# Optimization experiments

Hardware: AMD Instinct MI355X
Metric: run time of the kernel (lower is better)

## Reference

```python
import jax, jax.numpy as jnp
import numpy as np

EPSILON = 1e-05


def setup_inputs() -> dict:
    key = jax.random.key(0)
    X = jax.random.normal(key, (4, 2048, 3), dtype=jnp.float32)
    K = jnp.ones((), dtype=jnp.float32)
    B = jnp.zeros((), dtype=jnp.float32)
    return {"X": X, "K": K, "B": B}


def reference(X, K, B):
    # X: [batch, N, D]
    delta_X = X[:, :, None, :] - X[:, None, :, :]          # [b, N, N, D]
    sq = jnp.sum(delta_X * delta_X, axis=-1, keepdims=True)  # [b, N, N, 1]
    # safe sqrt: distance is 0 on the diagonal; avoid nan-producing grad paths
    distance = jnp.sqrt(jnp.where(sq == 0, 1.0, sq))
    distance = jnp.where(sq == 0, 0.0, distance)
    direction = delta_X / (distance + EPSILON)
    force = (K * (distance - B)) * direction               # [b, N, N, D]
    aggregated_force = jnp.sum(force, axis=-2)             # [b, N, D]
    return X + aggregated_force
```

## Files before the change

kernel.cpp:

```cpp
#include <hip/hip_runtime.h>

#define NPTS 2048
#define NBATCH 4
#define TI 16
#define SJ 16
#define EPSF 1e-5f

__global__ __launch_bounds__(256) void spring_kernel(
    const float* __restrict__ X,
    const float* __restrict__ Kp,
    const float* __restrict__ Bp,
    float* __restrict__ out)
{
    __shared__ float xs[NPTS], ys[NPTS], zs[NPTS];

    const int tid = threadIdx.x;
    const int blocksPerBatch = NPTS / TI;
    const int b = blockIdx.x / blocksPerBatch;
    const int i_base = (blockIdx.x % blocksPerBatch) * TI;
    const float* Xb = X + b * (NPTS * 3);

    for (int e = tid; e < NPTS * 3; e += 256) {
        float v = Xb[e];
        int n = e / 3;
        int c = e - n * 3;
        if (c == 0)      xs[n] = v;
        else if (c == 1) ys[n] = v;
        else             zs[n] = v;
    }
    __syncthreads();

    const float K  = Kp[0];
    const float Bc = Bp[0];
    const float C  = K * (Bc + EPSF);

    const int il = tid >> 4;
    const int js = tid & 15;
    const int i  = i_base + il;

    const float xi = xs[i], yi = ys[i], zi = zs[i];

    float ax = 0.f, ay = 0.f, az = 0.f;
    #pragma unroll 8
    for (int j = js; j < NPTS; j += SJ) {
        float dx = xi - xs[j];
        float dy = yi - ys[j];
        float dz = zi - zs[j];
        float sq = dx*dx + dy*dy + dz*dz;
        float dist = __builtin_amdgcn_sqrtf(sq);
        float r = __builtin_amdgcn_rcpf(dist + EPSF);
        float s = fmaf(-C, r, K);
        ax = fmaf(dx, s, ax);
        ay = fmaf(dy, s, ay);
        az = fmaf(dz, s, az);
    }

    for (int d = 8; d > 0; d >>= 1) {
        ax += __shfl_down(ax, d, 16);
        ay += __shfl_down(ay, d, 16);
        az += __shfl_down(az, d, 16);
    }

    if (js == 0) {
        float* o = out + (b * NPTS + i) * 3;
        o[0] = xi + ax;
        o[1] = yi + ay;
        o[2] = zi + az;
    }
}

extern "C" void kernel_launch(void* const* d_in, const int* in_sizes, int n_in,
                              void* d_out, int out_size, void* d_ws, size_t ws_size,
                              hipStream_t stream) {
    const float* X  = (const float*)d_in[0];
    const float* Kp = (const float*)d_in[1];
    const float* Bp = (const float*)d_in[2];
    float* out = (float*)d_out;

    dim3 grid(NBATCH * (NPTS / TI));
    dim3 block(256);
    spring_kernel<<<grid, block, 0, stream>>>(X, Kp, Bp, out);
}
```

Before: 67.66 us.

## Use rsq-based force with vectorized float4 shared-memory reads

Replaces the sqrt plus reciprocal per pair with a single reciprocal square root by dropping the epsilon in the denominator and clamping the squared distance. Shared-memory loads of neighbor coordinates become float4 reads covering four points per load, so fewer LDS instructions are issued. The force formula changes slightly (epsilon handling), which introduces tiny numerical differences versus the reference.

```diff
diff --git a/kernel.cpp b/kernel.cpp
--- a/kernel.cpp
+++ b/kernel.cpp
@@ -1,9 +1,6 @@
 #include <hip/hip_runtime.h>
 
 #define NPTS 2048
-#define NBATCH 4
-#define TI 16
-#define SJ 16
 #define EPSF 1e-5f
 
 __global__ __launch_bounds__(256) void spring_kernel(
@@ -12,13 +9,14 @@
     const float* __restrict__ Bp,
     float* __restrict__ out)
 {
-    __shared__ float xs[NPTS], ys[NPTS], zs[NPTS];
+    __shared__ __align__(16) float xs[NPTS];
+    __shared__ __align__(16) float ys[NPTS];
+    __shared__ __align__(16) float zs[NPTS];
 
-    const int tid = threadIdx.x;
-    const int blocksPerBatch = NPTS / TI;
-    const int b = blockIdx.x / blocksPerBatch;
-    const int i_base = (blockIdx.x % blocksPerBatch) * TI;
-    const float* Xb = X + b * (NPTS * 3);
+    const int tid    = threadIdx.x;
+    const int b      = blockIdx.x >> 7;
+    const int i_base = (blockIdx.x & 127) << 4;
+    const float* Xb  = X + b * (NPTS * 3);
 
     for (int e = tid; e < NPTS * 3; e += 256) {
         float v = Xb[e];
@@ -31,8 +29,7 @@
     __syncthreads();
 
     const float K  = Kp[0];
-    const float Bc = Bp[0];
-    const float C  = K * (Bc + EPSF);
+    const float KB = K * Bp[0];
 
     const int il = tid >> 4;
     const int js = tid & 15;
@@ -40,19 +37,35 @@
 
     const float xi = xs[i], yi = ys[i], zi = zs[i];
 
+    const float4* xs4 = (const float4*)xs;
+    const float4* ys4 = (const float4*)ys;
+    const float4* zs4 = (const float4*)zs;
+
     float ax = 0.f, ay = 0.f, az = 0.f;
-    #pragma unroll 8
-    for (int j = js; j < NPTS; j += SJ) {
-        float dx = xi - xs[j];
-        float dy = yi - ys[j];
-        float dz = zi - zs[j];
-        float sq = dx*dx + dy*dy + dz*dz;
-        float dist = __builtin_amdgcn_sqrtf(sq);
-        float r = __builtin_amdgcn_rcpf(dist + EPSF);
-        float s = fmaf(-C, r, K);
-        ax = fmaf(dx, s, ax);
-        ay = fmaf(dy, s, ay);
-        az = fmaf(dz, s, az);
+
+    #pragma unroll 4
+    for (int t = 0; t < NPTS / 4 / 16; ++t) {
+        const int idx = t * 16 + js;
+        float4 jx = xs4[idx];
+        float4 jy = ys4[idx];
+        float4 jz = zs4[idx];
+
+        #define PAIR(cx, cy, cz)                                   \
+        {                                                          \
+            float dx = xi - (cx), dy = yi - (cy), dz = zi - (cz);  \
+            float sq = fmaf(dx, dx, fmaf(dy, dy, dz * dz));        \
+            sq = fmaxf(sq, 1e-30f);      \
+            float r = __builtin_amdgcn_rsqf(sq);                   \
+            float s = fmaf(-KB, r, K);              \
+            ax = fmaf(dx, s, ax);                                  \
+            ay = fmaf(dy, s, ay);                                  \
+            az = fmaf(dz, s, az);                                  \
+        }
+        PAIR(jx.x, jy.x, jz.x)
+        PAIR(jx.y, jy.y, jz.y)
+        PAIR(jx.z, jy.z, jz.z)
+        PAIR(jx.w, jy.w, jz.w)
+        #undef PAIR
     }
 
     for (int d = 8; d > 0; d >>= 1) {
@@ -77,7 +90,7 @@
     const float* Bp = (const float*)d_in[2];
     float* out = (float*)d_out;
 
-    dim3 grid(NBATCH * (NPTS / TI));
+    dim3 grid(4 * (NPTS / 16));
     dim3 block(256);
     spring_kernel<<<grid, block, 0, stream>>>(X, Kp, Bp, out);
 }
```

New measurement: 66.99 us. Within noise of the previous version (-1.0%).
